# Performance work log

Hardware: AMD Instinct MI355X
Metric: run time of the kernel (lower is better)

Reference implementation:

```python
import jax, jax.numpy as jnp
import numpy as np


def setup_inputs() -> dict:
    key = jax.random.key(0)
    ks = jax.random.split(key, 6)
    B, L, NC = 32, 10000, 80
    REG_MAX, K, HID = 32, 4, 64
    IN = 4 * (K + 1)  # 20
    scores = jax.random.normal(ks[0], (B, L, NC), dtype=jnp.float32)
    pred_corners = jax.random.normal(ks[1], (B, L, 4 * (REG_MAX + 1)), dtype=jnp.float32)
    w1 = jax.random.normal(ks[2], (HID, IN), dtype=jnp.float32) * (1.0 / np.sqrt(IN))
    b1 = jax.random.normal(ks[3], (HID,), dtype=jnp.float32) * 0.01
    w2 = jax.random.normal(ks[4], (1, HID), dtype=jnp.float32) * (1.0 / np.sqrt(HID))
    b2 = jax.random.normal(ks[5], (1,), dtype=jnp.float32) * 0.01
    return {"scores": scores, "pred_corners": pred_corners,
            "w1": w1, "b1": b1, "w2": w2, "b2": b2, "k_top": K}


def reference(scores, pred_corners, w1, b1, w2, b2, k_top):
    B, L, D = pred_corners.shape
    nbins = D // 4  # reg_max + 1
    # softmax over the distribution bins of each of the 4 box sides
    prob = jax.nn.softmax(pred_corners.reshape(B, L, 4, nbins), axis=-1)
    prob_topk, _ = jax.lax.top_k(prob, k_top)                      # [B, L, 4, k]
    stat = jnp.concatenate(
        [prob_topk, prob_topk.mean(axis=-1, keepdims=True)], axis=-1)  # [B, L, 4, k+1]
    stat = stat.reshape(B, L, 4 * (k_top + 1))                     # [B, L, 4*(k+1)]
    # tiny MLP: Linear -> ReLU -> Linear
    h = jax.nn.relu(jnp.einsum('bli,hi->blh', stat, w1) + b1)      # [B, L, hid]
    quality = jnp.einsum('blh,oh->blo', h, w2) + b2                # [B, L, 1]
    return scores + quality
```

## Files before the change

### kernel.cpp

```cpp
#include <hip/hip_runtime.h>
#include <cstdint>
#include <cmath>


constexpr int NB   = 33;
constexpr int DPR  = 132;
constexpr int HID  = 64;
constexpr int NCLS = 80;
constexpr int APB  = 64;

#define AS_GLOBAL __attribute__((address_space(1)))
#define AS_LDS    __attribute__((address_space(3)))

__device__ __forceinline__ void dma16(const void* g, void* l) {
    __builtin_amdgcn_global_load_lds((const AS_GLOBAL uint32_t*)g,
                                     (AS_LDS uint32_t*)l, 16, 0, 0);
}

__global__
__attribute__((amdgpu_flat_work_group_size(APB, APB), amdgpu_waves_per_eu(1, 4)))
void lqe_fused(
    const float* __restrict__ scores,
    const float* __restrict__ pred,
    const float* __restrict__ w1,
    const float* __restrict__ b1,
    const float* __restrict__ w2,
    const float* __restrict__ b2,
    float* __restrict__ out)
{
    __shared__ float s_pred[APB * DPR];
    __shared__ float s_w1[HID * 16];
    __shared__ float s_b1[HID];
    __shared__ float s_w2[HID];
    __shared__ float s_b2;
    __shared__ float s_q[APB];

    const int t = threadIdx.x;
    const long long ab = (long long)blockIdx.x * APB;

    {
        const uint32_t* g = (const uint32_t*)pred + ab * DPR;
        uint32_t* l = (uint32_t*)s_pred;
        #pragma unroll
        for (int k = 0; k < 33; ++k)
            dma16(g + k * 256 + t * 4,
                  l + k * 256);
    }

    {
        #pragma unroll
        for (int s = 0; s < 4; ++s) {
            float wm = 0.25f * w1[t * 20 + s * 5 + 4];
            #pragma unroll
            for (int q = 0; q < 4; ++q)
                s_w1[t * 16 + s * 4 + q] = w1[t * 20 + s * 5 + q] + wm;
        }
        s_b1[t] = b1[t];
        s_w2[t] = w2[t];
        if (t == 0) s_b2 = b2[0];
    }

    __syncthreads();

    const float4* lp = (const float4*)(s_pred + t * DPR);

    float f[16];
    float e0 = 0.f, e1 = 0.f, e2 = 0.f, e3 = 0.f, sum = 0.f;

    #pragma unroll
    for (int ld = 0; ld < 33; ++ld) {
        float4 v4 = lp[ld];
        float vv[4] = {v4.x, v4.y, v4.z, v4.w};
        #pragma unroll
        for (int c = 0; c < 4; ++c) {
            const int idx = 4 * ld + c;
            float e = __expf(vv[c]);
            sum += e;
            float n0 = fminf(e0, e);  e0 = fmaxf(e0, e);
            float n1 = fminf(e1, n0); e1 = fmaxf(e1, n0);
            float n2 = fminf(e2, n1); e2 = fmaxf(e2, n1);
            e3 = fmaxf(e3, n2);
            if (idx % NB == NB - 1) {
                const int s = idx / NB;
                float inv = 1.0f / sum;
                f[s * 4 + 0] = e0 * inv;
                f[s * 4 + 1] = e1 * inv;
                f[s * 4 + 2] = e2 * inv;
                f[s * 4 + 3] = e3 * inv;
                e0 = e1 = e2 = e3 = 0.f; sum = 0.f;
            }
        }
    }

    float qv = s_b2;
    #pragma unroll
    for (int j = 0; j < HID; ++j) {
        const float4* wr = (const float4*)(s_w1 + j * 16);
        float hj = s_b1[j];
        #pragma unroll
        for (int i4 = 0; i4 < 4; ++i4) {
            float4 w = wr[i4];
            hj = fmaf(f[4 * i4 + 0], w.x, hj);
            hj = fmaf(f[4 * i4 + 1], w.y, hj);
            hj = fmaf(f[4 * i4 + 2], w.z, hj);
            hj = fmaf(f[4 * i4 + 3], w.w, hj);
        }
        hj = fmaxf(hj, 0.f);
        qv = fmaf(hj, s_w2[j], qv);
    }

    s_q[t] = qv;
    __syncthreads();

    const float4* sc4 = (const float4*)(scores + ab * NCLS);
    float4*       ot4 = (float4*)(out + ab * NCLS);

    float4 v[20];
    float  q[20];
    #pragma unroll
    for (int u = 0; u < 20; ++u) {
        const int i = u * APB + t;
        v[u] = sc4[i];
        q[u] = s_q[i / 20];
    }
    #pragma unroll
    for (int u = 0; u < 20; ++u) {
        const int i = u * APB + t;
        float4 w = v[u];
        w.x += q[u]; w.y += q[u]; w.z += q[u]; w.w += q[u];
        ot4[i] = w;
    }
}

extern "C" void kernel_launch(void* const* d_in, const int* in_sizes, int n_in,
                              void* d_out, int out_size, void* d_ws, size_t ws_size,
                              hipStream_t stream) {
    const float* scores = (const float*)d_in[0];
    const float* pred   = (const float*)d_in[1];
    const float* w1     = (const float*)d_in[2];
    const float* b1     = (const float*)d_in[3];
    const float* w2     = (const float*)d_in[4];
    const float* b2     = (const float*)d_in[5];

    int n_anchor = in_sizes[0] / NCLS;
    int blocks   = n_anchor / APB;
    lqe_fused<<<blocks, APB, 0, stream>>>(scores, pred, w1, b1, w2, b2,
                                          (float*)d_out);
}
```

Baseline: 348.6 us.

## Process five anchor tiles per block with double-buffered LDS prefetch of predictions

Each block now handles five 64-anchor tiles instead of one. Prediction tiles are staged into two LDS buffers with async global-to-LDS loads and explicit vmcnt waits, so the softmax/top-k/MLP compute of one tile overlaps the load of the next. The per-block weight setup is amortized over the five tiles. In exchange the grid shrinks fivefold and LDS per block roughly doubles, which cuts resident waves and overall memory parallelism. The score/output pass also runs serially per tile afterward.

```diff
diff --git a/kernel.cpp b/kernel.cpp
--- a/kernel.cpp
+++ b/kernel.cpp
@@ -8,6 +8,7 @@
 constexpr int HID  = 64;
 constexpr int NCLS = 80;
 constexpr int APB  = 64;
+constexpr int TPB  = 5;
 
 #define AS_GLOBAL __attribute__((address_space(1)))
 #define AS_LDS    __attribute__((address_space(3)))
@@ -18,7 +19,7 @@
 }
 
 __global__
-__attribute__((amdgpu_flat_work_group_size(APB, APB), amdgpu_waves_per_eu(1, 4)))
+__attribute__((amdgpu_flat_work_group_size(APB, APB), amdgpu_waves_per_eu(1, 2)))
 void lqe_fused(
     const float* __restrict__ scores,
     const float* __restrict__ pred,
@@ -28,107 +29,127 @@
     const float* __restrict__ b2,
     float* __restrict__ out)
 {
-    __shared__ float s_pred[APB * DPR];
+    __shared__ float s_pred[2][APB * DPR];
     __shared__ float s_w1[HID * 16];
     __shared__ float s_b1[HID];
     __shared__ float s_w2[HID];
-    __shared__ float s_b2;
-    __shared__ float s_q[APB];
+    __shared__ float s_q[TPB][APB];
 
     const int t = threadIdx.x;
-    const long long ab = (long long)blockIdx.x * APB;
+    const long long tile0 = (long long)blockIdx.x * TPB;
+    const long long ab0   = tile0 * APB;
 
+    float wreg[20];
     {
-        const uint32_t* g = (const uint32_t*)pred + ab * DPR;
-        uint32_t* l = (uint32_t*)s_pred;
+        const float4* wsrc = (const float4*)(w1 + t * 20);
+        #pragma unroll
+        for (int i = 0; i < 5; ++i) ((float4*)wreg)[i] = wsrc[i];
+    }
+    const float b1r = b1[t];
+    const float w2r = w2[t];
+    const float b2r = b2[0];
+
+    #pragma unroll
+    for (int s = 0; s < 4; ++s) {
+        float wm = 0.25f * wreg[s * 5 + 4];
+        #pragma unroll
+        for (int q = 0; q < 4; ++q)
+            s_w1[t * 16 + s * 4 + q] = wreg[s * 5 + q] + wm;
+    }
+    s_b1[t] = b1r;
+    s_w2[t] = w2r;
+
+    auto stage = [&](int slot, long long tile) {
+        const uint32_t* g = (const uint32_t*)pred + tile * (long long)(APB * DPR);
+        uint32_t* l = (uint32_t*)&s_pred[slot][0];
         #pragma unroll
         for (int k = 0; k < 33; ++k)
-            dma16(g + k * 256 + t * 4,
-                  l + k * 256);
+            dma16(g + k * 256 + t * 4, l + k * 256);
+    };
+
+    auto process = [&](const float* buf, int row) {
+        const float4* lp = (const float4*)(buf + t * DPR);
+        float f[16];
+        float e0 = 0.f, e1 = 0.f, e2 = 0.f, e3 = 0.f, sum = 0.f;
+        #pragma unroll
+        for (int ld = 0; ld < 33; ++ld) {
+            float4 v4 = lp[ld];
+            float vv[4] = {v4.x, v4.y, v4.z, v4.w};
+            #pragma unroll
+            for (int c = 0; c < 4; ++c) {
+                const int idx = 4 * ld + c;
+                float e = __expf(vv[c]);
+                sum += e;
+                float n0 = fminf(e0, e);  e0 = fmaxf(e0, e);
+                float n1 = fminf(e1, n0); e1 = fmaxf(e1, n0);
+                float n2 = fminf(e2, n1); e2 = fmaxf(e2, n1);
+                e3 = fmaxf(e3, n2);
+                if (idx % NB == NB - 1) {
+                    const int s = idx / NB;
+                    float inv = 1.0f / sum;
+                    f[s * 4 + 0] = e0 * inv;
+                    f[s * 4 + 1] = e1 * inv;
+                    f[s * 4 + 2] = e2 * inv;
+                    f[s * 4 + 3] = e3 * inv;
+                    e0 = e1 = e2 = e3 = 0.f; sum = 0.f;
+                }
+            }
+        }
+        float qv = b2r;
+        #pragma unroll
+        for (int j = 0; j < HID; ++j) {
+            const float4* wr = (const float4*)(s_w1 + j * 16);
+            float hj = s_b1[j];
+            #pragma unroll
+            for (int i4 = 0; i4 < 4; ++i4) {
+                float4 w = wr[i4];
+                hj = fmaf(f[4 * i4 + 0], w.x, hj);
+                hj = fmaf(f[4 * i4 + 1], w.y, hj);
+                hj = fmaf(f[4 * i4 + 2], w.z, hj);
+                hj = fmaf(f[4 * i4 + 3], w.w, hj);
+            }
+            hj = fmaxf(hj, 0.f);
+            qv = fmaf(hj, s_w2[j], qv);
+        }
+        s_q[row][t] = qv;
+    };
+
+    stage(0, tile0 + 0);
+    stage(1, tile0 + 1);
+
+    #pragma unroll
+    for (int i = 0; i < TPB; ++i) {
+        if (i < TPB - 1)
+            asm volatile("s_waitcnt vmcnt(33)" ::: "memory");
+        else
+            asm volatile("s_waitcnt vmcnt(0)"  ::: "memory");
+        process(&s_pred[i & 1][0], i);
+        asm volatile("s_waitcnt lgkmcnt(0)" ::: "memory");
+        if (i + 2 < TPB)
+            stage(i & 1, tile0 + i + 2);
     }
 
-    {
+    #pragma unroll 1
+    for (int i = 0; i < TPB; ++i) {
+        const long long ab = ab0 + (long long)i * APB;
+        const float4* sc4 = (const float4*)(scores + ab * NCLS);
+        float4*       ot4 = (float4*)(out + ab * NCLS);
+        float4 v[20];
+        float  q[20];
         #pragma unroll
-        for (int s = 0; s < 4; ++s) {
-            float wm = 0.25f * w1[t * 20 + s * 5 + 4];
-            #pragma unroll
-            for (int q = 0; q < 4; ++q)
-                s_w1[t * 16 + s * 4 + q] = w1[t * 20 + s * 5 + q] + wm;
+        for (int u = 0; u < 20; ++u) {
+            const int idx = u * APB + t;
+            v[u] = sc4[idx];
+            q[u] = s_q[i][idx / 20];
         }
-        s_b1[t] = b1[t];
-        s_w2[t] = w2[t];
-        if (t == 0) s_b2 = b2[0];
-    }
-
-    __syncthreads();
-
-    const float4* lp = (const float4*)(s_pred + t * DPR);
-
-    float f[16];
-    float e0 = 0.f, e1 = 0.f, e2 = 0.f, e3 = 0.f, sum = 0.f;
-
-    #pragma unroll
-    for (int ld = 0; ld < 33; ++ld) {
-        float4 v4 = lp[ld];
-        float vv[4] = {v4.x, v4.y, v4.z, v4.w};
         #pragma unroll
-        for (int c = 0; c < 4; ++c) {
-            const int idx = 4 * ld + c;
-            float e = __expf(vv[c]);
-            sum += e;
-            float n0 = fminf(e0, e);  e0 = fmaxf(e0, e);
-            float n1 = fminf(e1, n0); e1 = fmaxf(e1, n0);
-            float n2 = fminf(e2, n1); e2 = fmaxf(e2, n1);
-            e3 = fmaxf(e3, n2);
-            if (idx % NB == NB - 1) {
-                const int s = idx / NB;
-                float inv = 1.0f / sum;
-                f[s * 4 + 0] = e0 * inv;
-                f[s * 4 + 1] = e1 * inv;
-                f[s * 4 + 2] = e2 * inv;
-                f[s * 4 + 3] = e3 * inv;
-                e0 = e1 = e2 = e3 = 0.f; sum = 0.f;
-            }
+        for (int u = 0; u < 20; ++u) {
+            const int idx = u * APB + t;
+            float4 w = v[u];
+            float qq = q[u];
+            w.x += qq; w.y += qq; w.z += qq; w.w += qq;
+            ot4[idx] = w;
         }
-    }
-
-    float qv = s_b2;
-    #pragma unroll
-    for (int j = 0; j < HID; ++j) {
-        const float4* wr = (const float4*)(s_w1 + j * 16);
-        float hj = s_b1[j];
-        #pragma unroll
-        for (int i4 = 0; i4 < 4; ++i4) {
-            float4 w = wr[i4];
-            hj = fmaf(f[4 * i4 + 0], w.x, hj);
-            hj = fmaf(f[4 * i4 + 1], w.y, hj);
-            hj = fmaf(f[4 * i4 + 2], w.z, hj);
-            hj = fmaf(f[4 * i4 + 3], w.w, hj);
-        }
-        hj = fmaxf(hj, 0.f);
-        qv = fmaf(hj, s_w2[j], qv);
-    }
-
-    s_q[t] = qv;
-    __syncthreads();
-
-    const float4* sc4 = (const float4*)(scores + ab * NCLS);
-    float4*       ot4 = (float4*)(out + ab * NCLS);
-
-    float4 v[20];
-    float  q[20];
-    #pragma unroll
-    for (int u = 0; u < 20; ++u) {
-        const int i = u * APB + t;
-        v[u] = sc4[i];
-        q[u] = s_q[i / 20];
-    }
-    #pragma unroll
-    for (int u = 0; u < 20; ++u) {
-        const int i = u * APB + t;
-        float4 w = v[u];
-        w.x += q[u]; w.y += q[u]; w.z += q[u]; w.w += q[u];
-        ot4[i] = w;
     }
 }
 
@@ -143,7 +164,7 @@
     const float* b2     = (const float*)d_in[5];
 
     int n_anchor = in_sizes[0] / NCLS;
-    int blocks   = n_anchor / APB;
+    int blocks   = n_anchor / (APB * TPB);
     lqe_fused<<<blocks, APB, 0, stream>>>(scores, pred, w1, b1, w2, b2,
                                           (float*)d_out);
 }
```

After: 416.3 us. 19.4% more time.

## Split fused kernel into quality-MLP kernel and separate broadcast-add kernel

Applied to the files above, without the earlier changes.

Un-fuses the kernel into two launches. The first computes the per-anchor quality value, with each 64-thread block looping over 5 tiles and staging pred through registers into LDS instead of global_load_lds DMA. The second is a wide 256-thread elementwise kernel that adds the quality from a workspace buffer to scores. The aim is a streaming add with better occupancy and less per-block weight-setup overhead, at the cost of an extra launch and a workspace round trip. Each tile's load is serialized behind a barrier with no overlap against compute.

```diff
diff --git a/kernel.cpp b/kernel.cpp
--- a/kernel.cpp
+++ b/kernel.cpp
@@ -5,131 +5,125 @@
 
 constexpr int NB   = 33;
 constexpr int DPR  = 132;
+constexpr int F4PA = 33;
 constexpr int HID  = 64;
 constexpr int NCLS = 80;
-constexpr int APB  = 64;
+constexpr int APT  = 64;
+constexpr int TPB  = 5;
 
-#define AS_GLOBAL __attribute__((address_space(1)))
-#define AS_LDS    __attribute__((address_space(3)))
-
-__device__ __forceinline__ void dma16(const void* g, void* l) {
-    __builtin_amdgcn_global_load_lds((const AS_GLOBAL uint32_t*)g,
-                                     (AS_LDS uint32_t*)l, 16, 0, 0);
-}
-
-__global__
-__attribute__((amdgpu_flat_work_group_size(APB, APB), amdgpu_waves_per_eu(1, 4)))
-void lqe_fused(
-    const float* __restrict__ scores,
+__global__ __attribute__((amdgpu_flat_work_group_size(64, 64)))
+void lqe_q(
     const float* __restrict__ pred,
     const float* __restrict__ w1,
     const float* __restrict__ b1,
     const float* __restrict__ w2,
     const float* __restrict__ b2,
-    float* __restrict__ out)
+    float* __restrict__ qout)
 {
-    __shared__ float s_pred[APB * DPR];
-    __shared__ float s_w1[HID * 16];
-    __shared__ float s_b1[HID];
-    __shared__ float s_w2[HID];
-    __shared__ float s_b2;
-    __shared__ float s_q[APB];
+    __shared__ float4 s_buf[APT * F4PA];
+    __shared__ float  s_w1[HID * 16];
+    __shared__ float  s_b1[HID];
+    __shared__ float  s_w2[HID];
 
     const int t = threadIdx.x;
-    const long long ab = (long long)blockIdx.x * APB;
 
     {
-        const uint32_t* g = (const uint32_t*)pred + ab * DPR;
-        uint32_t* l = (uint32_t*)s_pred;
+        float wr[20];
+        const float4* ws = (const float4*)(w1 + t * 20);
         #pragma unroll
-        for (int k = 0; k < 33; ++k)
-            dma16(g + k * 256 + t * 4,
-                  l + k * 256);
-    }
-
-    {
+        for (int i = 0; i < 5; ++i) ((float4*)wr)[i] = ws[i];
         #pragma unroll
         for (int s = 0; s < 4; ++s) {
-            float wm = 0.25f * w1[t * 20 + s * 5 + 4];
+            float wm = 0.25f * wr[s * 5 + 4];
             #pragma unroll
             for (int q = 0; q < 4; ++q)
-                s_w1[t * 16 + s * 4 + q] = w1[t * 20 + s * 5 + q] + wm;
+                s_w1[t * 16 + s * 4 + q] = wr[s * 5 + q] + wm;
         }
         s_b1[t] = b1[t];
         s_w2[t] = w2[t];
-        if (t == 0) s_b2 = b2[0];
     }
-
+    const float b2r = b2[0];
     __syncthreads();
 
-    const float4* lp = (const float4*)(s_pred + t * DPR);
+    const long long tile0 = (long long)blockIdx.x * TPB;
 
-    float f[16];
-    float e0 = 0.f, e1 = 0.f, e2 = 0.f, e3 = 0.f, sum = 0.f;
+    for (int i = 0; i < TPB; ++i) {
+        const long long tile = tile0 + i;
+        const float4* g4 = (const float4*)pred + tile * (APT * F4PA);
 
-    #pragma unroll
-    for (int ld = 0; ld < 33; ++ld) {
-        float4 v4 = lp[ld];
-        float vv[4] = {v4.x, v4.y, v4.z, v4.w};
         #pragma unroll
-        for (int c = 0; c < 4; ++c) {
-            const int idx = 4 * ld + c;
-            float e = __expf(vv[c]);
-            sum += e;
-            float n0 = fminf(e0, e);  e0 = fmaxf(e0, e);
-            float n1 = fminf(e1, n0); e1 = fmaxf(e1, n0);
-            float n2 = fminf(e2, n1); e2 = fmaxf(e2, n1);
-            e3 = fmaxf(e3, n2);
-            if (idx % NB == NB - 1) {
-                const int s = idx / NB;
-                float inv = 1.0f / sum;
-                f[s * 4 + 0] = e0 * inv;
-                f[s * 4 + 1] = e1 * inv;
-                f[s * 4 + 2] = e2 * inv;
-                f[s * 4 + 3] = e3 * inv;
-                e0 = e1 = e2 = e3 = 0.f; sum = 0.f;
+        for (int g = 0; g < 4; ++g) {
+            float4 r[8];
+            #pragma unroll
+            for (int j = 0; j < 8; ++j) r[j] = g4[(g * 8 + j) * 64 + t];
+            #pragma unroll
+            for (int j = 0; j < 8; ++j) s_buf[(g * 8 + j) * 64 + t] = r[j];
+        }
+        { float4 r = g4[32 * 64 + t]; s_buf[32 * 64 + t] = r; }
+
+        __syncthreads();
+
+        const float4* lp = (const float4*)s_buf + t * F4PA;
+        float f[16];
+        float e0 = 0.f, e1 = 0.f, e2 = 0.f, e3 = 0.f, sum = 0.f;
+        #pragma unroll
+        for (int ld = 0; ld < 33; ++ld) {
+            float4 v4 = lp[ld];
+            float vv[4] = {v4.x, v4.y, v4.z, v4.w};
+            #pragma unroll
+            for (int c = 0; c < 4; ++c) {
+                const int idx = 4 * ld + c;
+                float e = __expf(vv[c]);
+                sum += e;
+                float n0 = fminf(e0, e);  e0 = fmaxf(e0, e);
+                float n1 = fminf(e1, n0); e1 = fmaxf(e1, n0);
+                float n2 = fminf(e2, n1); e2 = fmaxf(e2, n1);
+                e3 = fmaxf(e3, n2);
+                if (idx % NB == NB - 1) {
+                    const int s = idx / NB;
+                    float inv = 1.0f / sum;
+                    f[s * 4 + 0] = e0 * inv;
+                    f[s * 4 + 1] = e1 * inv;
+                    f[s * 4 + 2] = e2 * inv;
+                    f[s * 4 + 3] = e3 * inv;
+                    e0 = e1 = e2 = e3 = 0.f; sum = 0.f;
+                }
             }
         }
+
+        float qv = b2r;
+        #pragma unroll
+        for (int j = 0; j < HID; ++j) {
+            const float4* wr = (const float4*)(s_w1 + j * 16);
+            float hj = s_b1[j];
+            #pragma unroll
+            for (int i4 = 0; i4 < 4; ++i4) {
+                float4 w = wr[i4];
+                hj = fmaf(f[4 * i4 + 0], w.x, hj);
+                hj = fmaf(f[4 * i4 + 1], w.y, hj);
+                hj = fmaf(f[4 * i4 + 2], w.z, hj);
+                hj = fmaf(f[4 * i4 + 3], w.w, hj);
+            }
+            hj = fmaxf(hj, 0.f);
+            qv = fmaf(hj, s_w2[j], qv);
+        }
+        qout[tile * APT + t] = qv;
+
+        __syncthreads();
     }
+}
 
-    float qv = s_b2;
-    #pragma unroll
-    for (int j = 0; j < HID; ++j) {
-        const float4* wr = (const float4*)(s_w1 + j * 16);
-        float hj = s_b1[j];
-        #pragma unroll
-        for (int i4 = 0; i4 < 4; ++i4) {
-            float4 w = wr[i4];
-            hj = fmaf(f[4 * i4 + 0], w.x, hj);
-            hj = fmaf(f[4 * i4 + 1], w.y, hj);
-            hj = fmaf(f[4 * i4 + 2], w.z, hj);
-            hj = fmaf(f[4 * i4 + 3], w.w, hj);
-        }
-        hj = fmaxf(hj, 0.f);
-        qv = fmaf(hj, s_w2[j], qv);
-    }
-
-    s_q[t] = qv;
-    __syncthreads();
-
-    const float4* sc4 = (const float4*)(scores + ab * NCLS);
-    float4*       ot4 = (float4*)(out + ab * NCLS);
-
-    float4 v[20];
-    float  q[20];
-    #pragma unroll
-    for (int u = 0; u < 20; ++u) {
-        const int i = u * APB + t;
-        v[u] = sc4[i];
-        q[u] = s_q[i / 20];
-    }
-    #pragma unroll
-    for (int u = 0; u < 20; ++u) {
-        const int i = u * APB + t;
-        float4 w = v[u];
-        w.x += q[u]; w.y += q[u]; w.z += q[u]; w.w += q[u];
-        ot4[i] = w;
-    }
+__global__ __launch_bounds__(256)
+void lqe_add(
+    const float* __restrict__ scores,
+    const float* __restrict__ qin,
+    float* __restrict__ out)
+{
+    const int i = blockIdx.x * 256 + threadIdx.x;
+    const float q = qin[i / 20];
+    float4 v = ((const float4*)scores)[i];
+    v.x += q; v.y += q; v.z += q; v.w += q;
+    ((float4*)out)[i] = v;
 }
 
 extern "C" void kernel_launch(void* const* d_in, const int* in_sizes, int n_in,
@@ -143,7 +137,10 @@
     const float* b2     = (const float*)d_in[5];
 
     int n_anchor = in_sizes[0] / NCLS;
-    int blocks   = n_anchor / APB;
-    lqe_fused<<<blocks, APB, 0, stream>>>(scores, pred, w1, b1, w2, b2,
-                                          (float*)d_out);
+    float* qbuf  = (float*)d_ws;
+
+    lqe_q<<<n_anchor / (APT * TPB), APT, 0, stream>>>(pred, w1, b1, w2, b2, qbuf);
+
+    int nf4 = n_anchor * (NCLS / 4);
+    lqe_add<<<nf4 / 256, 256, 0, stream>>>(scores, qbuf, (float*)d_out);
 }
```

New measurement: 351.9 us. About the same (+1.0%).
